# Kernel optimization log

Measured on AMD Instinct MI355X. Metric: run time of the kernel, lower is better.

Reference implementation:

```python
import jax, jax.numpy as jnp
import numpy as np
from jax import lax

B = 128      # graphs per batch
N = 68       # facial landmarks (num_nodes per graph)
C = 3        # input channels
P = 32       # PATCH_SIZE
K = 16       # NUM_KERNELS
FD = 64      # feature_dim
GH = 128     # gcn_hidden_dim
OUT = 2      # output_dim
EG = 8 * N   # edges per graph
T = B * N    # total nodes


def setup_inputs() -> dict:
    key = jax.random.key(0)
    ks = jax.random.split(key, 8)
    x = jax.random.normal(ks[0], (T, C, P, P), jnp.float32)
    e = jax.random.randint(ks[1], (2, B, EG), 0, N)
    offs = (jnp.arange(B) * N)[None, :, None]
    edge_index = (e + offs).reshape(2, -1)            # within-graph edges, global ids
    batch = jnp.repeat(jnp.arange(B), N)              # node -> graph id
    conv_w = jax.random.normal(ks[2], (N, K, C, 3, 3), jnp.float32) * 0.05
    conv_b = jnp.zeros((N, K), jnp.float32)
    lin1_w = jax.random.normal(ks[3], (N, K * (P // 2) * (P // 2), FD), jnp.float32) * 0.02
    lin1_b = jnp.zeros((N, FD), jnp.float32)
    gcn_w = jax.random.normal(ks[4], (FD, GH), jnp.float32) * 0.1
    gcn_b = jnp.zeros((GH,), jnp.float32)
    mlp_w1 = jax.random.normal(ks[5], (GH, GH // 2), jnp.float32) * 0.1
    mlp_b1 = jnp.zeros((GH // 2,), jnp.float32)
    mlp_w2 = jax.random.normal(ks[6], (GH // 2, OUT), jnp.float32) * 0.1
    mlp_b2 = jnp.zeros((OUT,), jnp.float32)
    return dict(x=x, edge_index=edge_index, batch=batch, conv_w=conv_w, conv_b=conv_b,
                lin1_w=lin1_w, lin1_b=lin1_b, gcn_w=gcn_w, gcn_b=gcn_b,
                mlp_w1=mlp_w1, mlp_b1=mlp_b1, mlp_w2=mlp_w2, mlp_b2=mlp_b2)


def reference(x, edge_index, batch, conv_w, conv_b, lin1_w, lin1_b,
              gcn_w, gcn_b, mlp_w1, mlp_b1, mlp_w2, mlp_b2):
    # --- per-node-type CNN routing (nodes are laid out [graph, local_index]) ---
    xr = x.reshape(B, N, C, P, P)

    def cnn_one(xn, w, b):           # xn: [B,C,P,P]  w: [K,C,3,3]
        y = lax.conv_general_dilated(xn, w, (1, 1), 'SAME',
                                     dimension_numbers=('NCHW', 'OIHW', 'NCHW'))
        return jax.nn.relu(y + b[None, :, None, None])

    a = jax.vmap(cnn_one, in_axes=(1, 0, 0), out_axes=1)(xr, conv_w, conv_b)  # [B,N,K,P,P]
    pooled = lax.reduce_window(a, -jnp.inf, lax.max,
                               (1, 1, 1, 2, 2), (1, 1, 1, 2, 2), 'VALID')     # [B,N,K,P/2,P/2]
    flat = pooled.reshape(B, N, -1)
    feats = jax.nn.relu(jnp.einsum('bnf,nfo->bno', flat, lin1_w) + lin1_b[None])  # [B,N,FD]
    nodes = feats.reshape(T, FD)

    # --- GCNConv: add self-loops, symmetric normalization ---
    loop = jnp.arange(T)
    src = jnp.concatenate([edge_index[0], loop])
    dst = jnp.concatenate([edge_index[1], loop])
    deg = jax.ops.segment_sum(jnp.ones_like(dst, jnp.float32), dst, T)
    dis = jnp.where(deg > 0, 1.0 / jnp.sqrt(deg), 0.0)
    norm = dis[src] * dis[dst]
    xw = nodes @ gcn_w                                   # [T,GH]
    h = jax.ops.segment_sum(norm[:, None] * xw[src], dst, T) + gcn_b
    h = jax.nn.relu(h)

    # --- global mean pool over graphs ---
    cnt = jax.ops.segment_sum(jnp.ones((T,), jnp.float32), batch, B)
    g = jax.ops.segment_sum(h, batch, B) / cnt[:, None]  # [B,GH]

    # --- MLP head ---
    z = jax.nn.relu(g @ mlp_w1 + mlp_b1)
    return z @ mlp_w2 + mlp_b2                           # [B,OUT]
```

## Files before the change

kernel.cpp:

```cpp
#include <hip/hip_runtime.h>
#include <hip/hip_fp16.h>

#define B_   128
#define N_   68
#define C_   3
#define P_   32
#define K_   16
#define FD_  64
#define GH_  128
#define EG_  544
#define T_   8704
#define FLAT_ 4096
#define FCH_ 16

typedef __attribute__((ext_vector_type(8))) _Float16 half8;
typedef __attribute__((ext_vector_type(2))) _Float16 half2v;
typedef __attribute__((ext_vector_type(4))) float   floatx4;
typedef __attribute__((ext_vector_type(2))) float   v2f;

__global__ __launch_bounds__(256, 3) void conv_pool_kernel(
    const float* __restrict__ x, const float* __restrict__ conv_w,
    const float* __restrict__ conv_b, _Float16* __restrict__ pooled) {
  const int t = blockIdx.x;
  const int n = t % N_;
  const int tid = threadIdx.x;

  __shared__ float xs[3 * 34 * 34];
  __shared__ float wS[K_ * 28];

  {
    const float* wp = conv_w + (size_t)n * (K_ * 27);
    const float* bp = conv_b + (size_t)n * K_;
    for (int i = tid; i < K_ * 28; i += 256) {
      int k = i / 28, j = i - k * 28;
      wS[i] = (j < 27) ? wp[k * 27 + j] : bp[k];
    }
  }
  for (int i = tid; i < 396; i += 256) {
    int c = i / 132, j = i - c * 132;
    int off;
    if (j < 34)       off = j;
    else if (j < 68)  off = 33 * 34 + (j - 34);
    else if (j < 100) off = (j - 68 + 1) * 34;
    else              off = (j - 100 + 1) * 34 + 33;
    xs[c * 1156 + off] = 0.0f;
  }
  const float4* xg = (const float4*)(x + (size_t)t * (C_ * P_ * P_));
  #pragma unroll
  for (int j = 0; j < 3; j++) {
    int i4 = tid + j * 256;
    float4 v = xg[i4];
    int f0 = i4 * 4;
    int c = f0 >> 10, rem = f0 & 1023, y = rem >> 5, xc = rem & 31;
    float* dstp = &xs[c * 1156 + (y + 1) * 34 + xc + 1];
    dstp[0] = v.x; dstp[1] = v.y; dstp[2] = v.z; dstp[3] = v.w;
  }
  __syncthreads();

  const int py = tid >> 4, px = tid & 15;

  float xr[3][4][4];
  #pragma unroll
  for (int c = 0; c < 3; c++)
    #pragma unroll
    for (int r = 0; r < 4; r++)
      #pragma unroll
      for (int cc = 0; cc < 4; cc++)
        xr[c][r][cc] = xs[c * 1156 + (2 * py + r) * 34 + (2 * px + cc)];

  v2f vp[3][3][4];
  #pragma unroll
  for (int c = 0; c < 3; c++)
    #pragma unroll
    for (int rp = 0; rp < 3; rp++)
      #pragma unroll
      for (int col = 0; col < 4; col++)
        vp[c][rp][col] = (v2f){xr[c][rp][col], xr[c][rp + 1][col]};

  _Float16* outp = pooled + (size_t)t * FLAT_ + py * 16 + px;

  #pragma unroll 2
  for (int k = 0; k < K_; k++) {
    float w[28];
    const float4* wk4 = (const float4*)&wS[k * 28];
    #pragma unroll
    for (int q4 = 0; q4 < 7; q4++) *(float4*)&w[q4 * 4] = wk4[q4];
    float bk = w[27];
    v2f a0 = {bk, bk};
    v2f a1 = {bk, bk};
    #pragma unroll
    for (int c = 0; c < 3; c++)
      #pragma unroll
      for (int dy = 0; dy < 3; dy++)
        #pragma unroll
        for (int dx = 0; dx < 3; dx++) {
          float wsc = w[c * 9 + dy * 3 + dx];
          v2f wv = {wsc, wsc};
          a0 += vp[c][dy][dx]     * wv;
          a1 += vp[c][dy][dx + 1] * wv;
        }
    float m = fmaxf(fmaxf(a0.x, a0.y), fmaxf(a1.x, a1.y));
    m = fmaxf(m, 0.0f);
    outp[k * 256] = (_Float16)m;
  }
}

__global__ __launch_bounds__(256) void lin1_mfma_kernel(
    const _Float16* __restrict__ pooled, const float* __restrict__ lin1_w,
    float* __restrict__ part) {
  const int n   = blockIdx.x >> 4;
  const int fc  = blockIdx.x & 15;
  const int tid = threadIdx.x;
  const int wave = tid >> 6, lane = tid & 63;
  const int q = lane >> 4, lr = lane & 15;

  __shared__ __align__(16) _Float16 As[128 * 72];
  __shared__ __align__(16) _Float16 Bt[64 * 72];

  floatx4 acc[2][4];
  #pragma unroll
  for (int mt = 0; mt < 2; mt++)
    #pragma unroll
    for (int nt = 0; nt < 4; nt++)
      acc[mt][nt] = (floatx4){0.f, 0.f, 0.f, 0.f};

  const int f_base = fc * 256;
  const float* wbase = lin1_w + (size_t)n * (FLAT_ * FD_);

  uint4  aR[4];
  float4 bR[4];
  {
    const int f0 = f_base;
    #pragma unroll
    for (int j = 0; j < 4; j++) {
      int idx = tid + j * 256;
      int r = idx >> 3, ch = idx & 7;
      aR[j] = *(const uint4*)&pooled[(size_t)(r * N_ + n) * FLAT_ + f0 + ch * 8];
    }
    const float* wg = wbase + (size_t)f0 * FD_;
    #pragma unroll
    for (int it = 0; it < 2; it++) {
      int p = tid + it * 256;
      int o0 = (p & 15) * 4, k0 = (p >> 4) * 2;
      const float* wgk = wg + k0 * 64 + o0;
      bR[it * 2]     = *(const float4*)wgk;
      bR[it * 2 + 1] = *(const float4*)(wgk + 64);
    }
  }

  for (int step = 0; step < 4; step++) {
    #pragma unroll
    for (int j = 0; j < 4; j++) {
      int idx = tid + j * 256;
      int r = idx >> 3, ch = idx & 7;
      *(uint4*)&As[r * 72 + ch * 8] = aR[j];
    }
    #pragma unroll
    for (int it = 0; it < 2; it++) {
      int p = tid + it * 256;
      int o0 = (p & 15) * 4, k0 = (p >> 4) * 2;
      float4 va = bR[it * 2], vb = bR[it * 2 + 1];
      *(half2v*)&Bt[(o0 + 0) * 72 + k0] = (half2v){(_Float16)va.x, (_Float16)vb.x};
      *(half2v*)&Bt[(o0 + 1) * 72 + k0] = (half2v){(_Float16)va.y, (_Float16)vb.y};
      *(half2v*)&Bt[(o0 + 2) * 72 + k0] = (half2v){(_Float16)va.z, (_Float16)vb.z};
      *(half2v*)&Bt[(o0 + 3) * 72 + k0] = (half2v){(_Float16)va.w, (_Float16)vb.w};
    }
    __syncthreads();

    if (step < 3) {
      const int f0 = f_base + (step + 1) * 64;
      #pragma unroll
      for (int j = 0; j < 4; j++) {
        int idx = tid + j * 256;
        int r = idx >> 3, ch = idx & 7;
        aR[j] = *(const uint4*)&pooled[(size_t)(r * N_ + n) * FLAT_ + f0 + ch * 8];
      }
      const float* wg = wbase + (size_t)f0 * FD_;
      #pragma unroll
      for (int it = 0; it < 2; it++) {
        int p = tid + it * 256;
        int o0 = (p & 15) * 4, k0 = (p >> 4) * 2;
        const float* wgk = wg + k0 * 64 + o0;
        bR[it * 2]     = *(const float4*)wgk;
        bR[it * 2 + 1] = *(const float4*)(wgk + 64);
      }
    }

    #pragma unroll
    for (int kh = 0; kh < 2; kh++) {
      half8 af[2], bf[4];
      #pragma unroll
      for (int mt = 0; mt < 2; mt++)
        af[mt] = *(const half8*)&As[(wave * 32 + mt * 16 + lr) * 72 + kh * 32 + q * 8];
      #pragma unroll
      for (int nt = 0; nt < 4; nt++)
        bf[nt] = *(const half8*)&Bt[(nt * 16 + lr) * 72 + kh * 32 + q * 8];
      #pragma unroll
      for (int mt = 0; mt < 2; mt++)
        #pragma unroll
        for (int nt = 0; nt < 4; nt++)
          acc[mt][nt] = __builtin_amdgcn_mfma_f32_16x16x32_f16(
              af[mt], bf[nt], acc[mt][nt], 0, 0, 0);
    }
    __syncthreads();
  }

  float* pb = part + (size_t)fc * T_ * FD_;
  #pragma unroll
  for (int mt = 0; mt < 2; mt++) {
    #pragma unroll
    for (int v = 0; v < 4; v++) {
      int r = wave * 32 + mt * 16 + q * 4 + v;
      size_t base = (size_t)(r * N_ + n) * FD_;
      #pragma unroll
      for (int nt = 0; nt < 4; nt++)
        pb[base + nt * 16 + lr] = acc[mt][nt][v];
    }
  }
}

__global__ __launch_bounds__(512) void tail_kernel(
    const float* __restrict__ part, const int* __restrict__ edge_index,
    const float* __restrict__ lin1_b, const float* __restrict__ gcn_w,
    const float* __restrict__ gcn_b, const float* __restrict__ w1,
    const float* __restrict__ b1, const float* __restrict__ w2,
    const float* __restrict__ b2, float* __restrict__ out) {
  const int b = blockIdx.x;
  const int tid = threadIdx.x;

  __shared__ float fS[N_ * 68];
  __shared__ float aS[N_ * 68];
  __shared__ float wS[FD_ * GH_];
  __shared__ int   esrcS[EG_], edstS[EG_];
  __shared__ float nrmS[EG_];
  __shared__ int   degS[N_];
  __shared__ float disS[N_];
  __shared__ float gP[4][GH_];
  __shared__ float z1S[64];

  if (tid < N_) degS[tid] = 0;
  const int* srcp = edge_index;
  const int* dstp = edge_index + (B_ * EG_);
  const int e0 = b * EG_, nbase = b * N_;
  for (int e = tid; e < EG_; e += 512) {
    esrcS[e] = srcp[e0 + e] - nbase;
    edstS[e] = dstp[e0 + e] - nbase;
  }
  for (int idx4 = tid; idx4 < N_ * 16; idx4 += 512) {
    int i  = idx4 >> 4;
    int f4 = (idx4 & 15) * 4;
    int t  = b * N_ + i;
    float4 s = *(const float4*)&lin1_b[i * FD_ + f4];
    #pragma unroll
    for (int fc = 0; fc < FCH_; fc++) {
      float4 v = *(const float4*)&part[((size_t)fc * T_ + t) * FD_ + f4];
      s.x += v.x; s.y += v.y; s.z += v.z; s.w += v.w;
    }
    s.x = fmaxf(s.x, 0.f); s.y = fmaxf(s.y, 0.f);
    s.z = fmaxf(s.z, 0.f); s.w = fmaxf(s.w, 0.f);
    *(float4*)&fS[i * 68 + f4] = s;
  }
  #pragma unroll
  for (int j = 0; j < 4; j++)
    ((float4*)wS)[tid + j * 512] = ((const float4*)gcn_w)[tid + j * 512];
  __syncthreads();

  for (int e = tid; e < EG_; e += 512) atomicAdd(&degS[edstS[e]], 1);
  __syncthreads();
  if (tid < N_) disS[tid] = rsqrtf((float)(degS[tid] + 1));
  __syncthreads();
  for (int e = tid; e < EG_; e += 512)
    nrmS[e] = disS[esrcS[e]] * disS[edstS[e]];
  for (int idx4 = tid; idx4 < N_ * 16; idx4 += 512) {
    int i = idx4 >> 4, f4 = (idx4 & 15) * 4;
    float d2 = disS[i] * disS[i];
    float4 v = *(const float4*)&fS[i * 68 + f4];
    v.x *= d2; v.y *= d2; v.z *= d2; v.w *= d2;
    *(float4*)&aS[i * 68 + f4] = v;
  }
  __syncthreads();
  for (int idx = tid; idx < EG_ * FD_; idx += 512) {
    int e = idx >> 6, f = idx & 63;
    atomicAdd(&aS[edstS[e] * 68 + f], nrmS[e] * fS[esrcS[e] * 68 + f]);
  }
  __syncthreads();

  const int j = tid & 127, ig = tid >> 7;
  float wc[64];
  #pragma unroll
  for (int k = 0; k < 64; k++) wc[k] = wS[k * GH_ + j];
  const float bias = gcn_b[j];
  float gsum = 0.f;
  for (int i = ig; i < N_; i += 4) {
    float acc = bias;
    #pragma unroll
    for (int kq = 0; kq < 16; kq++) {
      float4 a = *(const float4*)&aS[i * 68 + kq * 4];
      acc += a.x * wc[kq * 4] + a.y * wc[kq * 4 + 1]
           + a.z * wc[kq * 4 + 2] + a.w * wc[kq * 4 + 3];
    }
    gsum += fmaxf(acc, 0.f);
  }
  gP[ig][j] = gsum;
  __syncthreads();
  if (tid < GH_)
    gP[0][tid] = (gP[0][tid] + gP[1][tid] + gP[2][tid] + gP[3][tid]) * (1.f / 68.f);
  __syncthreads();
  if (tid < 64) {
    float s = b1[tid];
    #pragma unroll 8
    for (int jj = 0; jj < GH_; jj++) s += gP[0][jj] * w1[jj * 64 + tid];
    z1S[tid] = fmaxf(s, 0.f);
  }
  __syncthreads();
  if (tid < 2) {
    float s = b2[tid];
    #pragma unroll 8
    for (int jj = 0; jj < 64; jj++) s += z1S[jj] * w2[jj * 2 + tid];
    out[b * 2 + tid] = s;
  }
}

extern "C" void kernel_launch(void* const* d_in, const int* in_sizes, int n_in,
                              void* d_out, int out_size, void* d_ws, size_t ws_size,
                              hipStream_t stream) {
  const float* x        = (const float*)d_in[0];
  const int*   edge_idx = (const int*)d_in[1];
  const float* conv_w   = (const float*)d_in[3];
  const float* conv_b   = (const float*)d_in[4];
  const float* lin1_w   = (const float*)d_in[5];
  const float* lin1_b   = (const float*)d_in[6];
  const float* gcn_w    = (const float*)d_in[7];
  const float* gcn_b    = (const float*)d_in[8];
  const float* mlp_w1   = (const float*)d_in[9];
  const float* mlp_b1   = (const float*)d_in[10];
  const float* mlp_w2   = (const float*)d_in[11];
  const float* mlp_b2   = (const float*)d_in[12];
  float* outp = (float*)d_out;

  char* wsb = (char*)d_ws;
  _Float16* pooled = (_Float16*)wsb;
  float* part  = (float*)(wsb + (size_t)T_ * FLAT_ * 2);

  conv_pool_kernel<<<T_, 256, 0, stream>>>(x, conv_w, conv_b, pooled);
  lin1_mfma_kernel<<<N_ * FCH_, 256, 0, stream>>>(pooled, lin1_w, part);
  tail_kernel<<<B_, 512, 0, stream>>>(part, edge_idx, lin1_b, gcn_w, gcn_b,
                                      mlp_w1, mlp_b1, mlp_w2, mlp_b2, outp);
}
```

Before: 375.6 us.

## Pre-transpose lin1 weights to fp16 and use LDS-free single-wave MFMA GEMM

```diff
diff --git a/kernel.cpp b/kernel.cpp
--- a/kernel.cpp
+++ b/kernel.cpp
@@ -14,11 +14,10 @@
 #define FCH_ 16
 
 typedef __attribute__((ext_vector_type(8))) _Float16 half8;
-typedef __attribute__((ext_vector_type(2))) _Float16 half2v;
 typedef __attribute__((ext_vector_type(4))) float   floatx4;
 typedef __attribute__((ext_vector_type(2))) float   v2f;
 
-__global__ __launch_bounds__(256, 3) void conv_pool_kernel(
+__global__ __launch_bounds__(256) void conv_pool_kernel(
     const float* __restrict__ x, const float* __restrict__ conv_w,
     const float* __restrict__ conv_b, _Float16* __restrict__ pooled) {
   const int t = blockIdx.x;
@@ -59,162 +58,132 @@
 
   const int py = tid >> 4, px = tid & 15;
 
-  float xr[3][4][4];
-  #pragma unroll
-  for (int c = 0; c < 3; c++)
+  v2f vp[3][3][4];
+  #pragma unroll
+  for (int c = 0; c < 3; c++) {
+    float tR[4][4];
     #pragma unroll
     for (int r = 0; r < 4; r++)
       #pragma unroll
       for (int cc = 0; cc < 4; cc++)
-        xr[c][r][cc] = xs[c * 1156 + (2 * py + r) * 34 + (2 * px + cc)];
-
-  v2f vp[3][3][4];
-  #pragma unroll
-  for (int c = 0; c < 3; c++)
+        tR[r][cc] = xs[c * 1156 + (2 * py + r) * 34 + (2 * px + cc)];
     #pragma unroll
     for (int rp = 0; rp < 3; rp++)
       #pragma unroll
       for (int col = 0; col < 4; col++)
-        vp[c][rp][col] = (v2f){xr[c][rp][col], xr[c][rp + 1][col]};
+        vp[c][rp][col] = (v2f){tR[rp][col], tR[rp + 1][col]};
+  }
 
   _Float16* outp = pooled + (size_t)t * FLAT_ + py * 16 + px;
 
   #pragma unroll 2
   for (int k = 0; k < K_; k++) {
-    float w[28];
     const float4* wk4 = (const float4*)&wS[k * 28];
-    #pragma unroll
-    for (int q4 = 0; q4 < 7; q4++) *(float4*)&w[q4 * 4] = wk4[q4];
-    float bk = w[27];
+    float bk = wS[k * 28 + 27];
     v2f a0 = {bk, bk};
     v2f a1 = {bk, bk};
     #pragma unroll
-    for (int c = 0; c < 3; c++)
+    for (int g = 0; g < 7; g++) {
+      float4 wq = wk4[g];
       #pragma unroll
-      for (int dy = 0; dy < 3; dy++)
-        #pragma unroll
-        for (int dx = 0; dx < 3; dx++) {
-          float wsc = w[c * 9 + dy * 3 + dx];
+      for (int e = 0; e < 4; e++) {
+        int idx = g * 4 + e;
+        if (idx < 27) {
+          int c = idx / 9, dy = (idx % 9) / 3, dx = idx % 3;
+          float wsc = (e == 0) ? wq.x : (e == 1) ? wq.y : (e == 2) ? wq.z : wq.w;
           v2f wv = {wsc, wsc};
           a0 += vp[c][dy][dx]     * wv;
           a1 += vp[c][dy][dx + 1] * wv;
         }
+      }
+    }
     float m = fmaxf(fmaxf(a0.x, a0.y), fmaxf(a1.x, a1.y));
     m = fmaxf(m, 0.0f);
     outp[k * 256] = (_Float16)m;
   }
 }
 
-__global__ __launch_bounds__(256) void lin1_mfma_kernel(
-    const _Float16* __restrict__ pooled, const float* __restrict__ lin1_w,
+__global__ __launch_bounds__(256) void wt_kernel(
+    const float* __restrict__ lin1_w, _Float16* __restrict__ wt) {
+  const int bid = blockIdx.x;
+  const int n  = bid >> 6;
+  const int k0 = (bid & 63) * 64;
+  const int tid = threadIdx.x;
+
+  __shared__ _Float16 tS[64 * 72];
+
+  #pragma unroll
+  for (int it = 0; it < 4; it++) {
+    int idx = tid + it * 256;
+    int krow = idx >> 4, o0 = (idx & 15) * 4;
+    float4 v = *(const float4*)&lin1_w[((size_t)n * FLAT_ + k0 + krow) * FD_ + o0];
+    tS[(o0 + 0) * 72 + krow] = (_Float16)v.x;
+    tS[(o0 + 1) * 72 + krow] = (_Float16)v.y;
+    tS[(o0 + 2) * 72 + krow] = (_Float16)v.z;
+    tS[(o0 + 3) * 72 + krow] = (_Float16)v.w;
+  }
+  __syncthreads();
+  #pragma unroll
+  for (int it = 0; it < 2; it++) {
+    int idx = tid + it * 256;
+    int o = idx >> 3, ch = idx & 7;
+    uint4 v = *(const uint4*)&tS[o * 72 + ch * 8];
+    *(uint4*)&wt[((size_t)(n * FD_ + o)) * FLAT_ + k0 + ch * 8] = v;
+  }
+}
+
+__global__ __launch_bounds__(64) void lin1_mfma_kernel(
+    const _Float16* __restrict__ pooled, const _Float16* __restrict__ wt,
     float* __restrict__ part) {
-  const int n   = blockIdx.x >> 4;
-  const int fc  = blockIdx.x & 15;
-  const int tid = threadIdx.x;
-  const int wave = tid >> 6, lane = tid & 63;
+  const int bid = blockIdx.x;
+  const int n  = bid >> 6;
+  const int fc = (bid >> 2) & 15;
+  const int rg = bid & 3;
+  const int lane = threadIdx.x;
   const int q = lane >> 4, lr = lane & 15;
 
-  __shared__ __align__(16) _Float16 As[128 * 72];
-  __shared__ __align__(16) _Float16 Bt[64 * 72];
-
-  floatx4 acc[2][4];
-  #pragma unroll
-  for (int mt = 0; mt < 2; mt++)
-    #pragma unroll
-    for (int nt = 0; nt < 4; nt++)
-      acc[mt][nt] = (floatx4){0.f, 0.f, 0.f, 0.f};
-
+  const int r0 = rg * 32;
   const int f_base = fc * 256;
-  const float* wbase = lin1_w + (size_t)n * (FLAT_ * FD_);
-
-  uint4  aR[4];
-  float4 bR[4];
-  {
-    const int f0 = f_base;
-    #pragma unroll
-    for (int j = 0; j < 4; j++) {
-      int idx = tid + j * 256;
-      int r = idx >> 3, ch = idx & 7;
-      aR[j] = *(const uint4*)&pooled[(size_t)(r * N_ + n) * FLAT_ + f0 + ch * 8];
-    }
-    const float* wg = wbase + (size_t)f0 * FD_;
-    #pragma unroll
-    for (int it = 0; it < 2; it++) {
-      int p = tid + it * 256;
-      int o0 = (p & 15) * 4, k0 = (p >> 4) * 2;
-      const float* wgk = wg + k0 * 64 + o0;
-      bR[it * 2]     = *(const float4*)wgk;
-      bR[it * 2 + 1] = *(const float4*)(wgk + 64);
-    }
-  }
-
-  for (int step = 0; step < 4; step++) {
-    #pragma unroll
-    for (int j = 0; j < 4; j++) {
-      int idx = tid + j * 256;
-      int r = idx >> 3, ch = idx & 7;
-      *(uint4*)&As[r * 72 + ch * 8] = aR[j];
-    }
-    #pragma unroll
-    for (int it = 0; it < 2; it++) {
-      int p = tid + it * 256;
-      int o0 = (p & 15) * 4, k0 = (p >> 4) * 2;
-      float4 va = bR[it * 2], vb = bR[it * 2 + 1];
-      *(half2v*)&Bt[(o0 + 0) * 72 + k0] = (half2v){(_Float16)va.x, (_Float16)vb.x};
-      *(half2v*)&Bt[(o0 + 1) * 72 + k0] = (half2v){(_Float16)va.y, (_Float16)vb.y};
-      *(half2v*)&Bt[(o0 + 2) * 72 + k0] = (half2v){(_Float16)va.z, (_Float16)vb.z};
-      *(half2v*)&Bt[(o0 + 3) * 72 + k0] = (half2v){(_Float16)va.w, (_Float16)vb.w};
-    }
-    __syncthreads();
-
-    if (step < 3) {
-      const int f0 = f_base + (step + 1) * 64;
+
+  floatx4 acc[4][2];
+  #pragma unroll
+  for (int mo = 0; mo < 4; mo++)
+    #pragma unroll
+    for (int nr = 0; nr < 2; nr++)
+      acc[mo][nr] = (floatx4){0.f, 0.f, 0.f, 0.f};
+
+  const _Float16* ap[4];
+  #pragma unroll
+  for (int mo = 0; mo < 4; mo++)
+    ap[mo] = wt + ((size_t)(n * FD_ + mo * 16 + lr)) * FLAT_ + f_base + q * 8;
+  const _Float16* bp[2];
+  #pragma unroll
+  for (int nr = 0; nr < 2; nr++)
+    bp[nr] = pooled + ((size_t)((r0 + nr * 16 + lr) * N_ + n)) * FLAT_ + f_base + q * 8;
+
+  #pragma unroll
+  for (int ks = 0; ks < 8; ks++) {
+    half8 av[4], bv[2];
+    #pragma unroll
+    for (int mo = 0; mo < 4; mo++) av[mo] = *(const half8*)(ap[mo] + ks * 32);
+    #pragma unroll
+    for (int nr = 0; nr < 2; nr++) bv[nr] = *(const half8*)(bp[nr] + ks * 32);
+    #pragma unroll
+    for (int mo = 0; mo < 4; mo++)
       #pragma unroll
-      for (int j = 0; j < 4; j++) {
-        int idx = tid + j * 256;
-        int r = idx >> 3, ch = idx & 7;
-        aR[j] = *(const uint4*)&pooled[(size_t)(r * N_ + n) * FLAT_ + f0 + ch * 8];
-      }
-      const float* wg = wbase + (size_t)f0 * FD_;
-      #pragma unroll
-      for (int it = 0; it < 2; it++) {
-        int p = tid + it * 256;
-        int o0 = (p & 15) * 4, k0 = (p >> 4) * 2;
-        const float* wgk = wg + k0 * 64 + o0;
-        bR[it * 2]     = *(const float4*)wgk;
-        bR[it * 2 + 1] = *(const float4*)(wgk + 64);
-      }
-    }
-
-    #pragma unroll
-    for (int kh = 0; kh < 2; kh++) {
-      half8 af[2], bf[4];
-      #pragma unroll
-      for (int mt = 0; mt < 2; mt++)
-        af[mt] = *(const half8*)&As[(wave * 32 + mt * 16 + lr) * 72 + kh * 32 + q * 8];
-      #pragma unroll
-      for (int nt = 0; nt < 4; nt++)
-        bf[nt] = *(const half8*)&Bt[(nt * 16 + lr) * 72 + kh * 32 + q * 8];
-      #pragma unroll
-      for (int mt = 0; mt < 2; mt++)
-        #pragma unroll
-        for (int nt = 0; nt < 4; nt++)
-          acc[mt][nt] = __builtin_amdgcn_mfma_f32_16x16x32_f16(
-              af[mt], bf[nt], acc[mt][nt], 0, 0, 0);
-    }
-    __syncthreads();
+      for (int nr = 0; nr < 2; nr++)
+        acc[mo][nr] = __builtin_amdgcn_mfma_f32_16x16x32_f16(
+            av[mo], bv[nr], acc[mo][nr], 0, 0, 0);
   }
 
   float* pb = part + (size_t)fc * T_ * FD_;
   #pragma unroll
-  for (int mt = 0; mt < 2; mt++) {
-    #pragma unroll
-    for (int v = 0; v < 4; v++) {
-      int r = wave * 32 + mt * 16 + q * 4 + v;
-      size_t base = (size_t)(r * N_ + n) * FD_;
-      #pragma unroll
-      for (int nt = 0; nt < 4; nt++)
-        pb[base + nt * 16 + lr] = acc[mt][nt][v];
+  for (int mo = 0; mo < 4; mo++) {
+    #pragma unroll
+    for (int nr = 0; nr < 2; nr++) {
+      int r = r0 + nr * 16 + lr;
+      int o = mo * 16 + q * 4;
+      *(floatx4*)&pb[(size_t)(r * N_ + n) * FD_ + o] = acc[mo][nr];
     }
   }
 }
@@ -340,10 +309,12 @@
 
   char* wsb = (char*)d_ws;
   _Float16* pooled = (_Float16*)wsb;
-  float* part  = (float*)(wsb + (size_t)T_ * FLAT_ * 2);
+  float*    part   = (float*)(wsb + (size_t)T_ * FLAT_ * 2);
+  _Float16* wtp    = (_Float16*)((char*)part + (size_t)FCH_ * T_ * FD_ * 4);
 
   conv_pool_kernel<<<T_, 256, 0, stream>>>(x, conv_w, conv_b, pooled);
-  lin1_mfma_kernel<<<N_ * FCH_, 256, 0, stream>>>(pooled, lin1_w, part);
+  wt_kernel<<<N_ * 64, 256, 0, stream>>>(lin1_w, wtp);
+  lin1_mfma_kernel<<<N_ * 64, 64, 0, stream>>>(pooled, wtp, part);
   tail_kernel<<<B_, 512, 0, stream>>>(part, edge_idx, lin1_b, gcn_w, gcn_b,
                                       mlp_w1, mlp_b1, mlp_w2, mlp_b2, outp);
 }
```

Measured after the change: 400.9 us. 6.7% more time.
